# Kernel optimization log

Measured on AMD Instinct MI355X. Metric: run time of the kernel, lower is better.

Reference implementation:

```python
import jax, jax.numpy as jnp
import numpy as np

B, IN, H, A = 2048, 2048, 2048, 2
DT = 0.05
TAU = 0.05
SIGMA_V = 1.0
V_RESET = 0.0
R = 0.1
I0 = 0.7


def setup_inputs() -> dict:
    key = jax.random.key(0)
    ks = jax.random.split(key, 13)
    return {
        "x": jax.random.normal(ks[0], (B, IN), jnp.float32),
        "firing": jax.random.uniform(ks[1], (B, H), jnp.float32),
        "voltage": jax.random.normal(ks[2], (B, H), jnp.float32),
        "ascurrent": jax.random.normal(ks[3], (A, B, H), jnp.float32),
        "syncurrent": jax.random.normal(ks[4], (B, H), jnp.float32),
        "firing_delayed": jax.random.uniform(ks[5], (B, H), jnp.float32),
        "weight_iv": jax.random.normal(ks[6], (IN, H), jnp.float32) / np.sqrt(H),
        "weight_lat": jax.random.normal(ks[7], (H, H), jnp.float32) / np.sqrt(H),
        "thresh": jax.random.normal(ks[8], (1, H), jnp.float32),
        "trans_k_m": jax.random.normal(ks[9], (1, H), jnp.float32),
        "trans_k_j": jax.random.normal(ks[10], (A, 1, H), jnp.float32),
        "trans_r_j": jax.random.normal(ks[11], (A, 1, H), jnp.float32),
        "a_j": jax.random.normal(ks[12], (A, 1, H), jnp.float32),
    }


def reference(x, firing, voltage, ascurrent, syncurrent, firing_delayed,
              weight_iv, weight_lat, thresh, trans_k_m, trans_k_j, trans_r_j, a_j):
    # synaptic current: input + lateral matmuls
    syncurrent = x @ weight_iv + firing_delayed @ weight_lat  # (B, H)
    # after-spike currents (broadcast params (A,1,H) over batch)
    asc_r = 1.0 - 2.0 * jax.nn.sigmoid(trans_r_j)
    k_j = jax.nn.sigmoid(trans_k_j) / DT
    ascurrent = ((ascurrent * asc_r + a_j) * firing * (DT / TAU)
                 + (1.0 - DT * k_j) * ascurrent)  # (A, B, H)
    # voltage update
    k_m = jax.nn.sigmoid(trans_k_m) / DT
    voltage = (syncurrent
               + DT * k_m * R * (jnp.sum(ascurrent, axis=0) + I0)
               + (1.0 - DT * k_m) * voltage
               - (DT / TAU) * firing * (voltage - V_RESET))
    # sigmoid spike function
    firing = jax.nn.sigmoid((voltage - thresh) / SIGMA_V)
    return (firing, voltage, ascurrent, syncurrent)
```

## Files before the change

### kernel.cpp

```cpp
#include <hip/hip_runtime.h>

typedef unsigned short u16;
typedef __bf16 __attribute__((ext_vector_type(8))) bf16x8;
typedef float __attribute__((ext_vector_type(4))) floatx4;

#define BH 4194304
#define HDIM 2048
#define KTOT 4096

__device__ __forceinline__ float bf2f(u16 u) {
  unsigned int v = ((unsigned int)u) << 16;
  return __builtin_bit_cast(float, v);
}
__device__ __forceinline__ u16 f2bf(float f) {
  unsigned int v = __builtin_bit_cast(unsigned int, f);
  unsigned int r = (v + 0x7fffu + ((v >> 16) & 1u)) >> 16;
  return (u16)r;
}
__device__ __forceinline__ unsigned cvtpk(float a, float b) {
  unsigned r;
  asm("v_cvt_pk_bf16_f32 %0, %1, %2" : "=v"(r) : "v"(a), "v"(b));
  return r;
}
__device__ __forceinline__ unsigned packu(u16 a, u16 b) {
  return (unsigned)a | ((unsigned)b << 16);
}
__device__ __forceinline__ float sigm(float x) {
  return 1.f / (1.f + __expf(-x));
}

template <bool F32> struct Elt { using T = float; };
template <> struct Elt<false> { using T = u16; };

template <bool F32> struct Stg;
template <> struct Stg<true>  { float4 a[2]; float b[8]; };
template <> struct Stg<false> { uint4  a;    u16   b[8]; };

template <bool F32>
__device__ __forceinline__ float ldel(const void* p, size_t i) {
  if constexpr (F32) return ((const float*)p)[i];
  else return bf2f(((const u16*)p)[i]);
}
template <bool F32>
__device__ __forceinline__ void stel(void* p, size_t i, float v) {
  if constexpr (F32) ((float*)p)[i] = v;
  else ((u16*)p)[i] = f2bf(v);
}

template <bool F32>
__device__ void glifr_body(
    const void* xv, const void* fdv, const void* wivv, const void* wlatv,
    const void* firingv, const void* voltagev, const void* ascv,
    const void* threshv, const void* tkmv, const void* tkjv,
    const void* trjv, const void* ajv, void* outv,
    u16* As, u16* Bs) {
  using El = typename Elt<F32>::T;
  const El* x    = (const El*)xv;
  const El* fd   = (const El*)fdv;
  const El* wiv  = (const El*)wivv;
  const El* wlat = (const El*)wlatv;

  const int tid  = threadIdx.x;
  const int lane = tid & 63;
  const int w    = tid >> 6;
  const int wm   = w >> 2;
  const int wn   = w & 3;
  const int m0   = blockIdx.y * 64;
  const int n0   = blockIdx.x * 64;

  const int rowA = tid >> 3;
  const int dgA  = tid & 7;
  const int quad = lane >> 4;
  const int col  = lane & 15;
  const int kbase = w * 8;

  floatx4 acc[2] = {};
  Stg<F32> S;

  auto issueA = [&](const El* asrc) {
    const El* p = asrc + (size_t)(m0 + rowA) * HDIM + dgA * 8;
    if constexpr (F32) {
      S.a[0] = *(const float4*)p;
      S.a[1] = *(const float4*)(p + 4);
    } else {
      S.a = *(const uint4*)p;
    }
  };
  auto issueB = [&](const El* wsrc) {
    const El* p = wsrc + (size_t)kbase * HDIM + n0 + lane;
#pragma unroll
    for (int j = 0; j < 8; ++j) S.b[j] = p[(size_t)j * HDIM];
  };
  auto writeTile = [&]() {
    uint4 qa;
    if constexpr (F32) {
      qa.x = cvtpk(S.a[0].x, S.a[0].y);
      qa.y = cvtpk(S.a[0].z, S.a[0].w);
      qa.z = cvtpk(S.a[1].x, S.a[1].y);
      qa.w = cvtpk(S.a[1].z, S.a[1].w);
    } else {
      qa = S.a;
    }
    *(uint4*)&As[rowA * 64 + ((dgA ^ (rowA & 7)) << 3)] = qa;
    uint4 qb;
    if constexpr (F32) {
      qb.x = cvtpk(S.b[0], S.b[1]);
      qb.y = cvtpk(S.b[2], S.b[3]);
      qb.z = cvtpk(S.b[4], S.b[5]);
      qb.w = cvtpk(S.b[6], S.b[7]);
    } else {
      qb.x = packu(S.b[0], S.b[1]);
      qb.y = packu(S.b[2], S.b[3]);
      qb.z = packu(S.b[4], S.b[5]);
      qb.w = packu(S.b[6], S.b[7]);
    }
    *(uint4*)&Bs[lane * 64 + ((w ^ (lane & 7)) << 3)] = qb;
  };
  auto mfmaPhase = [&]() {
#pragma unroll
    for (int kk = 0; kk < 64; kk += 32) {
      bf16x8 af[2], bf;
#pragma unroll
      for (int mi = 0; mi < 2; ++mi) {
        const int r = wm * 32 + mi * 16 + col;
        const int p = ((kk >> 3) + quad) ^ (r & 7);
        af[mi] = *(const bf16x8*)&As[r * 64 + p * 8];
      }
      {
        const int r = wn * 16 + col;
        const int p = ((kk >> 3) + quad) ^ (r & 7);
        bf = *(const bf16x8*)&Bs[r * 64 + p * 8];
      }
#pragma unroll
      for (int mi = 0; mi < 2; ++mi)
        acc[mi] = __builtin_amdgcn_mfma_f32_16x16x32_bf16(
            af[mi], bf, acc[mi], 0, 0, 0);
    }
  };
  auto srcA = [&](int kn) -> const El* {
    return (kn < 2048) ? (x + kn) : (fd + (kn - 2048));
  };
  auto srcW = [&](int kn) -> const El* {
    return (kn < 2048) ? (wiv + (size_t)kn * HDIM)
                       : (wlat + (size_t)(kn - 2048) * HDIM);
  };

  issueA(srcA(0));
  issueB(srcW(0));

  for (int kb = 0; kb < KTOT; kb += 64) {
    writeTile();
    if (kb + 64 < KTOT) {
      issueA(srcA(kb + 64));
      issueB(srcW(kb + 64));
    }
    __syncthreads();
    mfmaPhase();
    __syncthreads();
  }

  {
    const int h = n0 + wn * 16 + col;
    const float th  = ldel<F32>(threshv, h);
    const float sm  = sigm(ldel<F32>(tkmv, h));
    const float sk0 = sigm(ldel<F32>(tkjv, h));
    const float sk1 = sigm(ldel<F32>(tkjv, HDIM + h));
    const float r0  = 1.f - 2.f * sigm(ldel<F32>(trjv, h));
    const float r1  = 1.f - 2.f * sigm(ldel<F32>(trjv, HDIM + h));
    const float a0c = ldel<F32>(ajv, h);
    const float a1c = ldel<F32>(ajv, HDIM + h);
#pragma unroll
    for (int mi = 0; mi < 2; ++mi) {
#pragma unroll
      for (int i = 0; i < 4; ++i) {
        const int m = m0 + wm * 32 + mi * 16 + quad * 4 + i;
        const size_t idx = (size_t)m * HDIM + h;
        const float f   = ldel<F32>(firingv, idx);
        const float v   = ldel<F32>(voltagev, idx);
        const float A0  = ldel<F32>(ascv, idx);
        const float A1  = ldel<F32>(ascv, BH + idx);
        const float syn = acc[mi][i];
        const float na0 = (A0 * r0 + a0c) * f + (1.f - sk0) * A0;
        const float na1 = (A1 * r1 + a1c) * f + (1.f - sk1) * A1;
        const float nv  = syn + sm * 0.1f * (na0 + na1 + 0.7f)
                          + (1.f - sm) * v - f * v;
        const float nf  = sigm(nv - th);
        stel<F32>(outv, idx,            nf);
        stel<F32>(outv, BH + idx,       nv);
        stel<F32>(outv, 2 * BH + idx,   na0);
        stel<F32>(outv, 3 * BH + idx,   na1);
        stel<F32>(outv, 4 * BH + idx,   syn);
      }
    }
  }
}

__device__ __forceinline__ bool detect_f32(const u16* xu) {
  bool wild = false;
  for (int i = (threadIdx.x & 63); i < 1024; i += 64) {
    const u16 u = xu[i];
    if ((u & 0x7f80u) == 0x7f80u || fabsf(bf2f(u)) > 64.f) wild = true;
  }
  return __any(wild);
}

__global__ __launch_bounds__(512, 8) void glifr_fused(
    const void* x, const void* fd, const void* wiv, const void* wlat,
    const void* firing, const void* voltage, const void* asc,
    const void* thresh, const void* tkm, const void* tkj, const void* trj,
    const void* aj, void* out) {
  __shared__ u16 As[64 * 64];
  __shared__ u16 Bs[64 * 64];
  if (detect_f32((const u16*)x)) {
    glifr_body<true>(x, fd, wiv, wlat, firing, voltage, asc, thresh, tkm,
                     tkj, trj, aj, out, As, Bs);
  } else {
    glifr_body<false>(x, fd, wiv, wlat, firing, voltage, asc, thresh, tkm,
                      tkj, trj, aj, out, As, Bs);
  }
}

extern "C" void kernel_launch(void* const* d_in, const int* in_sizes, int n_in,
                              void* d_out, int out_size, void* d_ws, size_t ws_size,
                              hipStream_t stream) {
  const void* x    = d_in[0];
  const void* fir  = d_in[1];
  const void* vol  = d_in[2];
  const void* asc  = d_in[3];
  const void* fd   = d_in[5];
  const void* wiv  = d_in[6];
  const void* wlat = d_in[7];
  const void* th   = d_in[8];
  const void* tkm  = d_in[9];
  const void* tkj  = d_in[10];
  const void* trj  = d_in[11];
  const void* aj   = d_in[12];

  glifr_fused<<<dim3(32, 32), 512, 0, stream>>>(
      x, fd, wiv, wlat, fir, vol, asc, th, tkm, tkj, trj, aj, d_out);
}
```

Baseline: 328.1 us.

## Double-buffer LDS tiles to drop one barrier per K step

Switches the GEMM main loop from a single shared-memory A/B tile to ping-pong buffers. The next tile is written into the alternate buffer while MFMAs read the current one, so each 64-wide K step needs one __syncthreads instead of two. This doubles LDS use per block (32 KB), which may reduce how many blocks fit per CU.

```diff
diff --git a/kernel.cpp b/kernel.cpp
--- a/kernel.cpp
+++ b/kernel.cpp
@@ -53,7 +53,7 @@
     const void* firingv, const void* voltagev, const void* ascv,
     const void* threshv, const void* tkmv, const void* tkjv,
     const void* trjv, const void* ajv, void* outv,
-    u16* As, u16* Bs) {
+    u16* As0, u16* Bs0, u16* As1, u16* Bs1) {
   using El = typename Elt<F32>::T;
   const El* x    = (const El*)xv;
   const El* fd   = (const El*)fdv;
@@ -91,7 +91,7 @@
 #pragma unroll
     for (int j = 0; j < 8; ++j) S.b[j] = p[(size_t)j * HDIM];
   };
-  auto writeTile = [&]() {
+  auto writeTile = [&](u16* As, u16* Bs) {
     uint4 qa;
     if constexpr (F32) {
       qa.x = cvtpk(S.a[0].x, S.a[0].y);
@@ -116,7 +116,7 @@
     }
     *(uint4*)&Bs[lane * 64 + ((w ^ (lane & 7)) << 3)] = qb;
   };
-  auto mfmaPhase = [&]() {
+  auto mfmaPhase = [&](const u16* As, const u16* Bs) {
 #pragma unroll
     for (int kk = 0; kk < 64; kk += 32) {
       bf16x8 af[2], bf;
@@ -137,26 +137,34 @@
             af[mi], bf, acc[mi], 0, 0, 0);
     }
   };
-  auto srcA = [&](int kn) -> const El* {
+  auto srcA = [&](int ti) -> const El* {
+    const int kn = ti * 64;
     return (kn < 2048) ? (x + kn) : (fd + (kn - 2048));
   };
-  auto srcW = [&](int kn) -> const El* {
+  auto srcW = [&](int ti) -> const El* {
+    const int kn = ti * 64;
     return (kn < 2048) ? (wiv + (size_t)kn * HDIM)
                        : (wlat + (size_t)(kn - 2048) * HDIM);
   };
 
-  issueA(srcA(0));
-  issueB(srcW(0));
-
-  for (int kb = 0; kb < KTOT; kb += 64) {
-    writeTile();
-    if (kb + 64 < KTOT) {
-      issueA(srcA(kb + 64));
-      issueB(srcW(kb + 64));
-    }
-    __syncthreads();
-    mfmaPhase();
-    __syncthreads();
+  issueA(srcA(0));  issueB(srcW(0));
+  writeTile(As0, Bs0);
+  issueA(srcA(1));  issueB(srcW(1));
+  __syncthreads();
+
+  for (int ti = 0; ti < 64; ti += 2) {
+    {
+      mfmaPhase(As0, Bs0);
+      writeTile(As1, Bs1);
+      if (ti + 2 < 64) { issueA(srcA(ti + 2)); issueB(srcW(ti + 2)); }
+      __syncthreads();
+    }
+    {
+      mfmaPhase(As1, Bs1);
+      if (ti + 2 < 64) writeTile(As0, Bs0);
+      if (ti + 3 < 64) { issueA(srcA(ti + 3)); issueB(srcW(ti + 3)); }
+      __syncthreads();
+    }
   }
 
   {
@@ -209,14 +217,16 @@
     const void* firing, const void* voltage, const void* asc,
     const void* thresh, const void* tkm, const void* tkj, const void* trj,
     const void* aj, void* out) {
-  __shared__ u16 As[64 * 64];
-  __shared__ u16 Bs[64 * 64];
+  __shared__ u16 As0[64 * 64];
+  __shared__ u16 Bs0[64 * 64];
+  __shared__ u16 As1[64 * 64];
+  __shared__ u16 Bs1[64 * 64];
   if (detect_f32((const u16*)x)) {
     glifr_body<true>(x, fd, wiv, wlat, firing, voltage, asc, thresh, tkm,
-                     tkj, trj, aj, out, As, Bs);
+                     tkj, trj, aj, out, As0, Bs0, As1, Bs1);
   } else {
     glifr_body<false>(x, fd, wiv, wlat, firing, voltage, asc, thresh, tkm,
-                      tkj, trj, aj, out, As, Bs);
+                      tkj, trj, aj, out, As0, Bs0, As1, Bs1);
   }
 }
 
```

After: 331.9 us. Within noise of the previous version (+1.2%).

## Enlarge block tile to 128x64 with 2x2 MFMA per wave

Applied to the files above, without the earlier changes.

Doubles the M extent of each block tile from 64 to 128 rows. The wave layout changes from 2x4 to 4x2, and each wave now computes a 2x2 grid of 16x16 MFMA outputs instead of 2x1. This cuts redundant global loads of the weight B tiles and raises MFMA work per LDS read. The price is more registers, twice the A shared memory, half as many blocks, and a lower occupancy hint in the launch bounds.

```diff
diff --git a/kernel.cpp b/kernel.cpp
--- a/kernel.cpp
+++ b/kernel.cpp
@@ -33,8 +33,8 @@
 template <> struct Elt<false> { using T = u16; };
 
 template <bool F32> struct Stg;
-template <> struct Stg<true>  { float4 a[2]; float b[8]; };
-template <> struct Stg<false> { uint4  a;    u16   b[8]; };
+template <> struct Stg<true>  { float4 a[4]; float b[8]; };
+template <> struct Stg<false> { uint4  a[2]; u16   b[8]; };
 
 template <bool F32>
 __device__ __forceinline__ float ldel(const void* p, size_t i) {
@@ -63,9 +63,9 @@
   const int tid  = threadIdx.x;
   const int lane = tid & 63;
   const int w    = tid >> 6;
-  const int wm   = w >> 2;
-  const int wn   = w & 3;
-  const int m0   = blockIdx.y * 64;
+  const int wm   = w >> 1;
+  const int wn   = w & 1;
+  const int m0   = blockIdx.y * 128;
   const int n0   = blockIdx.x * 64;
 
   const int rowA = tid >> 3;
@@ -74,16 +74,19 @@
   const int col  = lane & 15;
   const int kbase = w * 8;
 
-  floatx4 acc[2] = {};
+  floatx4 acc[2][2] = {};
   Stg<F32> S;
 
   auto issueA = [&](const El* asrc) {
-    const El* p = asrc + (size_t)(m0 + rowA) * HDIM + dgA * 8;
-    if constexpr (F32) {
-      S.a[0] = *(const float4*)p;
-      S.a[1] = *(const float4*)(p + 4);
-    } else {
-      S.a = *(const uint4*)p;
+#pragma unroll
+    for (int s = 0; s < 2; ++s) {
+      const El* p = asrc + (size_t)(m0 + rowA + 64 * s) * HDIM + dgA * 8;
+      if constexpr (F32) {
+        S.a[2 * s]     = *(const float4*)p;
+        S.a[2 * s + 1] = *(const float4*)(p + 4);
+      } else {
+        S.a[s] = *(const uint4*)p;
+      }
     }
   };
   auto issueB = [&](const El* wsrc) {
@@ -92,16 +95,20 @@
     for (int j = 0; j < 8; ++j) S.b[j] = p[(size_t)j * HDIM];
   };
   auto writeTile = [&]() {
-    uint4 qa;
-    if constexpr (F32) {
-      qa.x = cvtpk(S.a[0].x, S.a[0].y);
-      qa.y = cvtpk(S.a[0].z, S.a[0].w);
-      qa.z = cvtpk(S.a[1].x, S.a[1].y);
-      qa.w = cvtpk(S.a[1].z, S.a[1].w);
-    } else {
-      qa = S.a;
-    }
-    *(uint4*)&As[rowA * 64 + ((dgA ^ (rowA & 7)) << 3)] = qa;
+#pragma unroll
+    for (int s = 0; s < 2; ++s) {
+      uint4 qa;
+      if constexpr (F32) {
+        qa.x = cvtpk(S.a[2 * s].x, S.a[2 * s].y);
+        qa.y = cvtpk(S.a[2 * s].z, S.a[2 * s].w);
+        qa.z = cvtpk(S.a[2 * s + 1].x, S.a[2 * s + 1].y);
+        qa.w = cvtpk(S.a[2 * s + 1].z, S.a[2 * s + 1].w);
+      } else {
+        qa = S.a[s];
+      }
+      const int r = rowA + 64 * s;
+      *(uint4*)&As[r * 64 + ((dgA ^ (r & 7)) << 3)] = qa;
+    }
     uint4 qb;
     if constexpr (F32) {
       qb.x = cvtpk(S.b[0], S.b[1]);
@@ -119,22 +126,25 @@
   auto mfmaPhase = [&]() {
 #pragma unroll
     for (int kk = 0; kk < 64; kk += 32) {
-      bf16x8 af[2], bf;
+      bf16x8 af[2], bf[2];
 #pragma unroll
       for (int mi = 0; mi < 2; ++mi) {
         const int r = wm * 32 + mi * 16 + col;
         const int p = ((kk >> 3) + quad) ^ (r & 7);
         af[mi] = *(const bf16x8*)&As[r * 64 + p * 8];
       }
-      {
-        const int r = wn * 16 + col;
+#pragma unroll
+      for (int ni = 0; ni < 2; ++ni) {
+        const int r = wn * 32 + ni * 16 + col;
         const int p = ((kk >> 3) + quad) ^ (r & 7);
-        bf = *(const bf16x8*)&Bs[r * 64 + p * 8];
+        bf[ni] = *(const bf16x8*)&Bs[r * 64 + p * 8];
       }
 #pragma unroll
       for (int mi = 0; mi < 2; ++mi)
-        acc[mi] = __builtin_amdgcn_mfma_f32_16x16x32_bf16(
-            af[mi], bf, acc[mi], 0, 0, 0);
+#pragma unroll
+        for (int ni = 0; ni < 2; ++ni)
+          acc[mi][ni] = __builtin_amdgcn_mfma_f32_16x16x32_bf16(
+              af[mi], bf[ni], acc[mi][ni], 0, 0, 0);
     }
   };
   auto srcA = [&](int kn) -> const El* {
@@ -159,8 +169,9 @@
     __syncthreads();
   }
 
-  {
-    const int h = n0 + wn * 16 + col;
+#pragma unroll
+  for (int ni = 0; ni < 2; ++ni) {
+    const int h = n0 + wn * 32 + ni * 16 + col;
     const float th  = ldel<F32>(threshv, h);
     const float sm  = sigm(ldel<F32>(tkmv, h));
     const float sk0 = sigm(ldel<F32>(tkjv, h));
@@ -179,7 +190,7 @@
         const float v   = ldel<F32>(voltagev, idx);
         const float A0  = ldel<F32>(ascv, idx);
         const float A1  = ldel<F32>(ascv, BH + idx);
-        const float syn = acc[mi][i];
+        const float syn = acc[mi][ni][i];
         const float na0 = (A0 * r0 + a0c) * f + (1.f - sk0) * A0;
         const float na1 = (A1 * r1 + a1c) * f + (1.f - sk1) * A1;
         const float nv  = syn + sm * 0.1f * (na0 + na1 + 0.7f)
@@ -204,12 +215,12 @@
   return __any(wild);
 }
 
-__global__ __launch_bounds__(512, 8) void glifr_fused(
+__global__ __launch_bounds__(512, 4) void glifr_fused(
     const void* x, const void* fd, const void* wiv, const void* wlat,
     const void* firing, const void* voltage, const void* asc,
     const void* thresh, const void* tkm, const void* tkj, const void* trj,
     const void* aj, void* out) {
-  __shared__ u16 As[64 * 64];
+  __shared__ u16 As[128 * 64];
   __shared__ u16 Bs[64 * 64];
   if (detect_f32((const u16*)x)) {
     glifr_body<true>(x, fd, wiv, wlat, firing, voltage, asc, thresh, tkm,
@@ -236,6 +247,6 @@
   const void* trj  = d_in[11];
   const void* aj   = d_in[12];
 
-  glifr_fused<<<dim3(32, 32), 512, 0, stream>>>(
+  glifr_fused<<<dim3(32, 16), 512, 0, stream>>>(
       x, fd, wiv, wlat, fir, vol, asc, th, tkm, tkj, trj, aj, d_out);
 }
```

New measurement: 344.1 us. 1.05x slower.
